# Kernel tuning notes

Measured on AMD Instinct MI355X. Metric: run time of the kernel, lower is better.

## Reference

```python
import jax, jax.numpy as jnp
import numpy as np

N_EMBED = 256
N_HEADS = 4
HEAD_SIZE = N_EMBED // N_HEADS  # 64
BLOCK_SIZE = 768
LN_EPS = 1e-5


def layer_norm(x, g, b):
    mu = jnp.mean(x, axis=-1, keepdims=True)
    var = jnp.var(x, axis=-1, keepdims=True)
    return (x - mu) * jax.lax.rsqrt(var + LN_EPS) * g + b


def setup_inputs() -> dict:
    key = jax.random.key(0)
    ks = jax.random.split(key, 12)
    B, T, C, H, hs = 32, BLOCK_SIZE, N_EMBED, N_HEADS, HEAD_SIZE
    s_in = 1.0 / np.sqrt(C)
    s_ff = 1.0 / np.sqrt(4 * C)
    return {
        "x": jax.random.normal(ks[0], (B, T, C), jnp.float32),
        # per-head projections, stacked: [H, C, hs]
        "Wq": jax.random.normal(ks[1], (H, C, hs), jnp.float32) * s_in,
        "Wk": jax.random.normal(ks[2], (H, C, hs), jnp.float32) * s_in,
        "Wv": jax.random.normal(ks[3], (H, C, hs), jnp.float32) * s_in,
        "Wo": jax.random.normal(ks[4], (C, C), jnp.float32) * s_in,
        "bo": jnp.zeros((C,), jnp.float32),
        "W1": jax.random.normal(ks[5], (C, 4 * C), jnp.float32) * s_in,
        "b1": jnp.zeros((4 * C,), jnp.float32),
        "W2": jax.random.normal(ks[6], (4 * C, C), jnp.float32) * s_ff,
        "b2": jnp.zeros((C,), jnp.float32),
        "g1": jnp.ones((C,), jnp.float32),
        "be1": jnp.zeros((C,), jnp.float32),
        "g2": jnp.ones((C,), jnp.float32),
        "be2": jnp.zeros((C,), jnp.float32),
    }


def reference(x, Wq, Wk, Wv, Wo, bo, W1, b1, W2, b2, g1, be1, g2, be2):
    B, T, C = x.shape
    # --- multi-head causal self-attention (pre-LN) ---
    h = layer_norm(x, g1, be1)
    q = jnp.einsum("btc,hcd->bhtd", h, Wq)
    k = jnp.einsum("btc,hcd->bhtd", h, Wk)
    v = jnp.einsum("btc,hcd->bhtd", h, Wv)
    scores = jnp.einsum("bhtd,bhsd->bhts", q, k) * (HEAD_SIZE ** -0.5)
    causal = jnp.tril(jnp.ones((T, T), bool))
    scores = jnp.where(causal, scores, -jnp.inf)
    attn = jax.nn.softmax(scores, axis=-1)  # dropout = identity (eval)
    o = jnp.einsum("bhts,bhsd->bhtd", attn, v)
    o = o.transpose(0, 2, 1, 3).reshape(B, T, C)  # concat heads
    x = x + o @ Wo + bo
    # --- feed-forward (pre-LN) ---
    h2 = layer_norm(x, g2, be2)
    x = x + jax.nn.relu(h2 @ W1 + b1) @ W2 + b2
    return x
```

## Files before the change

kernel.cpp:

```cpp
#include <hip/hip_runtime.h>
#include <stdint.h>

using short8   = __attribute__((ext_vector_type(8))) short;
using f32x4    = __attribute__((ext_vector_type(4))) float;
using ushort4v = __attribute__((ext_vector_type(4))) unsigned short;
using uint2v   = __attribute__((ext_vector_type(2))) unsigned int;

#define CSC  0.1803368801111f
#define FIXC 20.0f

__device__ __forceinline__ unsigned short f2bf(float f) {
    unsigned int u = __builtin_bit_cast(unsigned int, f);
    u += 0x7FFFu + ((u >> 16) & 1u);
    return (unsigned short)(u >> 16);
}
__device__ __forceinline__ float bf2f(unsigned short s) {
    unsigned int u = ((unsigned int)s) << 16;
    return __builtin_bit_cast(float, u);
}
__device__ __forceinline__ unsigned pk2bf(float a, float b) {
    unsigned r;
    asm("v_cvt_pk_bf16_f32 %0, %1, %2" : "=v"(r) : "v"(a), "v"(b));
    return r;
}

__device__ __forceinline__ void gload16(const void* g, void* l) {
    __builtin_amdgcn_global_load_lds(
        (const __attribute__((address_space(1))) void*)(uintptr_t)g,
        (__attribute__((address_space(3))) void*)(unsigned)(uintptr_t)l,
        16, 0, 0);
}

__device__ __forceinline__ uint2v ln_row_pk(f32x4 v, f32x4 gv, f32x4 bvv) {
    float s  = v[0] + v[1] + v[2] + v[3];
    float s2 = v[0]*v[0] + v[1]*v[1] + v[2]*v[2] + v[3]*v[3];
    for (int m = 1; m < 64; m <<= 1) {
        s  += __shfl_xor(s,  m, 64);
        s2 += __shfl_xor(s2, m, 64);
    }
    float mu  = s * (1.0f / 256.0f);
    float var = s2 * (1.0f / 256.0f) - mu * mu;
    float rs  = rsqrtf(var + 1e-5f);
    float r0 = (v[0] - mu) * rs * gv[0] + bvv[0];
    float r1 = (v[1] - mu) * rs * gv[1] + bvv[1];
    float r2 = (v[2] - mu) * rs * gv[2] + bvv[2];
    float r3 = (v[3] - mu) * rs * gv[3] + bvv[3];
    uint2v u; u[0] = pk2bf(r0, r1); u[1] = pk2bf(r2, r3);
    return u;
}

__global__ __launch_bounds__(256) void prep_k(const float* __restrict__ x, const float* __restrict__ g1,
                                              const float* __restrict__ be1, unsigned short* __restrict__ h,
                                              const float* __restrict__ Wq, const float* __restrict__ Wk,
                                              const float* __restrict__ Wv, const float* __restrict__ Wo,
                                              const float* __restrict__ W1, const float* __restrict__ W2,
                                              unsigned short* __restrict__ wpackT, unsigned short* __restrict__ woT,
                                              unsigned short* __restrict__ w1T, unsigned short* __restrict__ w2T) {
    __shared__ float t[64][65];
    if (blockIdx.x >= 192) {
        int row  = (blockIdx.x - 192) * 4 + (threadIdx.x >> 6);
        int lane = threadIdx.x & 63;
        f32x4 v = *(const f32x4*)(x + (size_t)row * 256 + lane * 4);
        f32x4 gv = *(const f32x4*)(g1 + lane * 4);
        f32x4 bv = *(const f32x4*)(be1 + lane * 4);
        uint2v u = ln_row_pk(v, gv, bv);
        *(uint2v*)(h + (size_t)row * 256 + lane * 4) = u;
        return;
    }
    const int bid = blockIdx.x;
    const float* in; unsigned short* out;
    int R, C, r0, c0;
    if (bid < 48) {
        int z = bid >> 2, cx = bid & 3;
        int qkv = z >> 2, hh = z & 3;
        in = ((qkv == 0) ? Wq : (qkv == 1) ? Wk : Wv) + (size_t)hh * 256 * 64;
        out = wpackT + (size_t)(qkv * 256 + hh * 64) * 256;
        R = 256; C = 64; r0 = cx * 64; c0 = 0;
    } else if (bid < 64) {
        int tt = bid - 48;
        in = Wo; out = woT; R = 256; C = 256; r0 = (tt >> 2) * 64; c0 = (tt & 3) * 64;
    } else if (bid < 128) {
        int tt = bid - 64;
        in = W1; out = w1T; R = 256; C = 1024; r0 = (tt & 3) * 64; c0 = (tt >> 2) * 64;
    } else {
        int tt = bid - 128;
        in = W2; out = w2T; R = 1024; C = 256; r0 = (tt & 15) * 64; c0 = (tt >> 4) * 64;
    }
    const int tx = threadIdx.x & 63, ty = threadIdx.x >> 6;
    #pragma unroll
    for (int i = 0; i < 64; i += 4)
        t[i + ty][tx] = in[(size_t)(r0 + i + ty) * C + c0 + tx];
    __syncthreads();
    #pragma unroll
    for (int i = 0; i < 64; i += 4)
        out[(size_t)(c0 + i + ty) * R + r0 + tx] = f2bf(t[tx][i + ty]);
}

__global__ __launch_bounds__(256) void qkv_k(const unsigned short* __restrict__ h,
                                             const unsigned short* __restrict__ wpackT,
                                             unsigned short* __restrict__ qk,
                                             unsigned short* __restrict__ vT) {
    __shared__ unsigned short As[128 * 64];
    __shared__ unsigned short Bs[128 * 64];
    const int tid  = threadIdx.x;
    const int lane = tid & 63;
    const int w    = tid >> 6;
    const int wm   = w >> 1, wn = w & 1;
    const int l15  = lane & 15, l4 = lane >> 4;
    const int bid  = blockIdx.x;

    const unsigned short *A, *BT;
    unsigned short* outp;
    int bm, bn, N;
    float qsc = 1.0f;
    if (bid < 768) {
        bn = bid & 3;  bm = bid >> 2;
        A = h; BT = wpackT; outp = qk; N = 512;
        if (bn < 2) qsc = CSC;
    } else {
        int t = bid - 768;
        bm = t & 1;    bn = t >> 1;
        A = wpackT + 512 * 256; BT = h; outp = vT; N = 24576;
    }
    const int K = 256;

    f32x4 acc[4][4] = {};

    const size_t K2 = (size_t)K * 2;
    const int i0   = w * 4096 + lane * 16;
    const int row0 = i0 >> 7;
    const int cb0  = (i0 & 127) ^ ((row0 & 7) << 4);
    const char* aSrc = (const char*)A  + ((size_t)(bm * 128 + row0)) * K2 + cb0;
    const char* bSrc = (const char*)BT + ((size_t)(bn * 128 + row0)) * K2 + cb0;

    for (int t = 0; t < 4; ++t) {
        {
            const char* aS = aSrc + (size_t)t * 128;
            const char* bS = bSrc + (size_t)t * 128;
            char* aD = (char*)&As[0] + w * 4096;
            char* bD = (char*)&Bs[0] + w * 4096;
            #pragma unroll
            for (int c = 0; c < 4; ++c) {
                gload16(aS + (size_t)c * 8 * K2, aD + c * 1024);
                gload16(bS + (size_t)c * 8 * K2, bD + c * 1024);
            }
        }
        __syncthreads();
        #pragma unroll
        for (int kf = 0; kf < 2; ++kf) {
            int kb = kf * 64 + l4 * 16;
            short8 af[4], bfr[4];
            #pragma unroll
            for (int mf = 0; mf < 4; ++mf) {
                int row = wm * 64 + mf * 16 + l15;
                af[mf] = *(const short8*)((const char*)&As[0] + ((row * 128 + kb) ^ ((row & 7) << 4)));
            }
            #pragma unroll
            for (int nf = 0; nf < 4; ++nf) {
                int row = wn * 64 + nf * 16 + l15;
                bfr[nf] = *(const short8*)((const char*)&Bs[0] + ((row * 128 + kb) ^ ((row & 7) << 4)));
            }
            #pragma unroll
            for (int mf = 0; mf < 4; ++mf)
                #pragma unroll
                for (int nf = 0; nf < 4; ++nf)
                    acc[mf][nf] = __builtin_amdgcn_mfma_f32_16x16x32_bf16(af[mf], bfr[nf], acc[mf][nf], 0, 0, 0);
        }
        __syncthreads();
    }

    #pragma unroll
    for (int nf = 0; nf < 4; ++nf) {
        int col = bn * 128 + wn * 64 + nf * 16 + l15;
        #pragma unroll
        for (int mf = 0; mf < 4; ++mf) {
            int row0o = bm * 128 + wm * 64 + mf * 16 + l4 * 4;
            size_t off = (size_t)row0o * N + col;
            unsigned p01 = pk2bf(acc[mf][nf][0] * qsc, acc[mf][nf][1] * qsc);
            unsigned p23 = pk2bf(acc[mf][nf][2] * qsc, acc[mf][nf][3] * qsc);
            outp[off]                 = (unsigned short)p01;
            outp[off + (size_t)N]     = (unsigned short)(p01 >> 16);
            outp[off + (size_t)N * 2] = (unsigned short)p23;
            outp[off + (size_t)N * 3] = (unsigned short)(p23 >> 16);
        }
    }
}

template <int EPI, bool DB>
__global__ __launch_bounds__(256) void gemm_bt(const unsigned short* __restrict__ A,
                                               const unsigned short* __restrict__ BT,
                                               void* __restrict__ outp,
                                               const float* __restrict__ bias,
                                               const void* __restrict__ resid,
                                               int K, int N) {
    __shared__ unsigned short As[DB ? 2 : 1][128 * 64];
    __shared__ unsigned short Bs[DB ? 2 : 1][128 * 64];
    const int tid  = threadIdx.x;
    const int lane = tid & 63;
    const int w    = tid >> 6;
    const int wm   = w >> 1, wn = w & 1;
    const int bm   = blockIdx.y, bn = blockIdx.x;
    const int l15  = lane & 15, l4 = lane >> 4;

    f32x4 acc[4][4] = {};

    const size_t K2 = (size_t)K * 2;
    const int i0   = w * 4096 + lane * 16;
    const int row0 = i0 >> 7;
    const int cb0  = (i0 & 127) ^ ((row0 & 7) << 4);
    const char* aSrc = (const char*)A  + ((size_t)(bm * 128 + row0)) * K2 + cb0;
    const char* bSrc = (const char*)BT + ((size_t)(bn * 128 + row0)) * K2 + cb0;
    const int nt = K >> 6;

    auto stage = [&](int t, int buf) {
        const char* aS = aSrc + (size_t)t * 128;
        const char* bS = bSrc + (size_t)t * 128;
        char* aD = (char*)&As[buf][0] + w * 4096;
        char* bD = (char*)&Bs[buf][0] + w * 4096;
        #pragma unroll
        for (int c = 0; c < 4; ++c) {
            gload16(aS + (size_t)c * 8 * K2, aD + c * 1024);
            gload16(bS + (size_t)c * 8 * K2, bD + c * 1024);
        }
    };
    auto compute = [&](int buf) {
        const char* AsB = (const char*)&As[buf][0];
        const char* BsB = (const char*)&Bs[buf][0];
        #pragma unroll
        for (int kf = 0; kf < 2; ++kf) {
            int kb = kf * 64 + l4 * 16;
            short8 af[4], bfr[4];
            #pragma unroll
            for (int mf = 0; mf < 4; ++mf) {
                int row = wm * 64 + mf * 16 + l15;
                af[mf] = *(const short8*)(AsB + ((row * 128 + kb) ^ ((row & 7) << 4)));
            }
            #pragma unroll
            for (int nf = 0; nf < 4; ++nf) {
                int row = wn * 64 + nf * 16 + l15;
                bfr[nf] = *(const short8*)(BsB + ((row * 128 + kb) ^ ((row & 7) << 4)));
            }
            #pragma unroll
            for (int mf = 0; mf < 4; ++mf)
                #pragma unroll
                for (int nf = 0; nf < 4; ++nf)
                    acc[mf][nf] = __builtin_amdgcn_mfma_f32_16x16x32_bf16(af[mf], bfr[nf], acc[mf][nf], 0, 0, 0);
        }
    };

    if (DB) {
        stage(0, 0);
        for (int t = 0; t < nt; ++t) {
            const int cur = t & 1;
            __syncthreads();
            if (t + 1 < nt) stage(t + 1, cur ^ 1);
            compute(cur);
        }
    } else {
        for (int t = 0; t < nt; ++t) {
            stage(t, 0);
            __syncthreads();
            compute(0);
            __syncthreads();
        }
    }

    #pragma unroll
    for (int nf = 0; nf < 4; ++nf) {
        int col = bn * 128 + wn * 64 + nf * 16 + l15;
        float bv = bias[col];
        #pragma unroll
        for (int mf = 0; mf < 4; ++mf) {
            int row0o = bm * 128 + wm * 64 + mf * 16 + l4 * 4;
            size_t off = (size_t)row0o * N + col;
            float v[4];
            #pragma unroll
            for (int r = 0; r < 4; ++r)
                v[r] = acc[mf][nf][r] + bv + ((const float*)resid)[off + (size_t)r * N];
            unsigned short* O = (unsigned short*)outp;
            unsigned p01 = pk2bf(v[0], v[1]), p23 = pk2bf(v[2], v[3]);
            O[off]                 = (unsigned short)p01;
            O[off + (size_t)N]     = (unsigned short)(p01 >> 16);
            O[off + (size_t)N * 2] = (unsigned short)p23;
            O[off + (size_t)N * 3] = (unsigned short)(p23 >> 16);
        }
    }
}

__global__ __launch_bounds__(256) void ff_fused(const unsigned short* __restrict__ x1b,
                                                const float* __restrict__ g2,
                                                const float* __restrict__ be2,
                                                const unsigned short* __restrict__ w1T,
                                                const unsigned short* __restrict__ w2T,
                                                const float* __restrict__ b1,
                                                const float* __restrict__ b2,
                                                float* __restrict__ out) {
    __shared__ unsigned short sA[4][64 * 64];
    __shared__ unsigned short sW[16384];
    __shared__ unsigned short sAct[64 * 64];
    const int tid = threadIdx.x, lane = tid & 63, w = tid >> 6;
    const int l15 = lane & 15, l4 = lane >> 4;
    const int wm = w >> 1, wn = w & 1;
    const int r0 = blockIdx.x * 64;

    {
        f32x4 gv = *(const f32x4*)(g2 + lane * 4);
        f32x4 bv = *(const f32x4*)(be2 + lane * 4);
        const int ks = lane >> 4, colb = (lane & 15) * 8;
        #pragma unroll
        for (int it = 0; it < 16; ++it) {
            int row = it * 4 + w;
            ushort4v u4 = *(const ushort4v*)(x1b + (size_t)(r0 + row) * 256 + lane * 4);
            f32x4 v;
            #pragma unroll
            for (int i = 0; i < 4; ++i) v[i] = bf2f(u4[i]);
            uint2v u = ln_row_pk(v, gv, bv);
            *(uint2v*)((char*)&sA[0][0] + ks * 8192 + row * 128 + (colb ^ ((row & 7) << 4))) = u;
        }
    }

    f32x4 oacc[2][8] = {};

    for (int c = 0; c < 16; ++c) {
        {
            const char* wb = (const char*)w1T + (size_t)(c * 64) * 512;
            #pragma unroll
            for (int g = 0; g < 8; ++g) {
                int j = g * 4096 + tid * 16;
                int ks = j >> 13, row = (j >> 7) & 63, cb = j & 127;
                gload16(wb + (size_t)row * 512 + ks * 128 + (cb ^ ((row & 7) << 4)),
                        (char*)&sW[0] + j);
            }
        }
        __syncthreads();

        f32x4 aacc[2][2] = {};
        __builtin_amdgcn_s_setprio(1);
        #pragma unroll
        for (int ks = 0; ks < 4; ++ks) {
            #pragma unroll
            for (int kf = 0; kf < 2; ++kf) {
                const int kb = kf * 64 + l4 * 16;
                short8 hf[2], wf[2];
                #pragma unroll
                for (int mf = 0; mf < 2; ++mf) {
                    int row = wm * 32 + mf * 16 + l15;
                    hf[mf] = *(const short8*)((const char*)&sA[ks][0] + ((row * 128 + kb) ^ ((row & 7) << 4)));
                }
                #pragma unroll
                for (int nf = 0; nf < 2; ++nf) {
                    int row = wn * 32 + nf * 16 + l15;
                    wf[nf] = *(const short8*)((const char*)&sW[ks * 4096] + ((row * 128 + kb) ^ ((row & 7) << 4)));
                }
                #pragma unroll
                for (int mf = 0; mf < 2; ++mf)
                    #pragma unroll
                    for (int nf = 0; nf < 2; ++nf)
                        aacc[mf][nf] = __builtin_amdgcn_mfma_f32_16x16x32_bf16(wf[nf], hf[mf], aacc[mf][nf], 0, 0, 0);
            }
        }
        __builtin_amdgcn_s_setprio(0);
        #pragma unroll
        for (int mf = 0; mf < 2; ++mf)
            #pragma unroll
            for (int nf = 0; nf < 2; ++nf) {
                int nl = wn * 32 + nf * 16 + l4 * 4;
                f32x4 bv = *(const f32x4*)(b1 + c * 64 + nl);
                float v0 = aacc[mf][nf][0] + bv[0]; v0 = v0 > 0.0f ? v0 : 0.0f;
                float v1 = aacc[mf][nf][1] + bv[1]; v1 = v1 > 0.0f ? v1 : 0.0f;
                float v2 = aacc[mf][nf][2] + bv[2]; v2 = v2 > 0.0f ? v2 : 0.0f;
                float v3 = aacc[mf][nf][3] + bv[3]; v3 = v3 > 0.0f ? v3 : 0.0f;
                uint2v u; u[0] = pk2bf(v0, v1); u[1] = pk2bf(v2, v3);
                int m = wm * 32 + mf * 16 + l15;
                *(uint2v*)((char*)&sAct[0] + ((m * 128 + nl * 2) ^ ((m & 7) << 4))) = u;
            }
        __syncthreads();

        {
            const char* wb = (const char*)w2T + (size_t)c * 128;
            #pragma unroll
            for (int g = 0; g < 8; ++g) {
                int j = g * 4096 + tid * 16;
                int row = j >> 7, cb = j & 127;
                gload16(wb + (size_t)row * 2048 + (cb ^ ((row & 7) << 4)),
                        (char*)&sW[0] + j);
            }
        }
        __syncthreads();

        __builtin_amdgcn_s_setprio(1);
        #pragma unroll
        for (int kf = 0; kf < 2; ++kf) {
            const int kb = kf * 64 + l4 * 16;
            short8 af[2], wf[8];
            #pragma unroll
            for (int mf = 0; mf < 2; ++mf) {
                int row = wm * 32 + mf * 16 + l15;
                af[mf] = *(const short8*)((const char*)&sAct[0] + ((row * 128 + kb) ^ ((row & 7) << 4)));
            }
            #pragma unroll
            for (int nf = 0; nf < 8; ++nf) {
                int row = wn * 128 + nf * 16 + l15;
                wf[nf] = *(const short8*)((const char*)&sW[0] + ((row * 128 + kb) ^ ((row & 7) << 4)));
            }
            #pragma unroll
            for (int mf = 0; mf < 2; ++mf)
                #pragma unroll
                for (int nf = 0; nf < 8; ++nf)
                    oacc[mf][nf] = __builtin_amdgcn_mfma_f32_16x16x32_bf16(af[mf], wf[nf], oacc[mf][nf], 0, 0, 0);
        }
        __builtin_amdgcn_s_setprio(0);
        __syncthreads();
    }

    #pragma unroll
    for (int nf = 0; nf < 8; ++nf) {
        const int col = wn * 128 + nf * 16 + l15;
        const float bv = b2[col];
        #pragma unroll
        for (int mf = 0; mf < 2; ++mf) {
            const int row = r0 + wm * 32 + mf * 16 + l4 * 4;
            const size_t off = (size_t)row * 256 + col;
            #pragma unroll
            for (int r = 0; r < 4; ++r)
                out[off + (size_t)r * 256] = oacc[mf][nf][r] + bv + bf2f(x1b[off + (size_t)r * 256]);
        }
    }
}

__global__ __launch_bounds__(256) void attn_k(const unsigned short* __restrict__ qk,
                                              const unsigned short* __restrict__ vT,
                                              unsigned short* __restrict__ o) {
    __shared__ unsigned short Ks[2][64 * 64];
    __shared__ unsigned short Vt[2][64 * 64];
    __shared__ unsigned short Pl[4][16 * 64];
    const int tid = threadIdx.x, lane = tid & 63, w = tid >> 6;
    const int l15 = lane & 15, l4 = lane >> 4;
    const int gid = blockIdx.x;
    const int xcd = gid & 7, slot = gid >> 3;
    const int sl6 = slot / 6;
    const int bh  = xcd * 16 + sl6;
    const int x   = slot - sl6 * 6;
    const int qb1 = x, qb2 = 11 - x;
    const int b = bh >> 2, h = bh & 3;
    const unsigned short* Qb = qk + (size_t)b * 768 * 512 + h * 64;
    const char* Kg = (const char*)(Qb + 256);
    const char* Vg = (const char*)(vT + (size_t)(h * 64) * 24576 + (size_t)b * 768);
    const int t01 = qb1 * 64, t02 = qb2 * 64;
    const int tq1 = t01 + w * 16 + l15;
    const int tq2 = t02 + w * 16 + l15;

    short8 q1f0 = *(const short8*)(Qb + (size_t)tq1 * 512 + l4 * 8);
    short8 q1f1 = *(const short8*)(Qb + (size_t)tq1 * 512 + 32 + l4 * 8);
    short8 q2f0 = *(const short8*)(Qb + (size_t)tq2 * 512 + l4 * 8);
    short8 q2f1 = *(const short8*)(Qb + (size_t)tq2 * 512 + 32 + l4 * 8);

    const int srow = w * 16 + (lane >> 3);
    const int scb  = ((lane & 7) * 16) ^ ((srow & 7) << 4);
    const char* kSrc = Kg + (size_t)srow * 1024 + scb;
    const char* vSrc = Vg + (size_t)srow * 49152 + scb;
    char* kDst0 = (char*)&Ks[0][0] + w * 2048;
    char* vDst0 = (char*)&Vt[0][0] + w * 2048;

    f32x4 oA[4] = {}, oB[4] = {};
    float lsA = 0.0f, lsB = 0.0f;
    unsigned short* Pw = &Pl[w][0];
    const char* KsB;
    const char* VtB;
    int sb = 0;

    auto do_tile = [&](short8 qf0, short8 qf1, f32x4 (&oacc)[4], float& lsum, bool diag, int tq) {
        f32x4 sacc[4] = {};
        __builtin_amdgcn_s_setprio(1);
        #pragma unroll
        for (int kf = 0; kf < 2; ++kf) {
            const int kb = kf * 64 + l4 * 16;
            short8 qf = kf ? qf1 : qf0;
            #pragma unroll
            for (int nf = 0; nf < 4; ++nf) {
                int sr = nf * 16 + l15;
                short8 kfr = *(const short8*)(KsB + ((sr * 128 + kb) ^ ((sr & 7) << 4)));
                sacc[nf] = __builtin_amdgcn_mfma_f32_16x16x32_bf16(kfr, qf, sacc[nf], 0, 0, 0);
            }
        }
        __builtin_amdgcn_s_setprio(0);

        if (diag) {
            #pragma unroll
            for (int nf = 0; nf < 4; ++nf)
                #pragma unroll
                for (int r = 0; r < 4; ++r) {
                    int s = sb * 64 + nf * 16 + l4 * 4 + r;
                    if (s > tq) sacc[nf][r] = -1e30f;
                }
        }
        float psum = 0.0f;
        #pragma unroll
        for (int nf = 0; nf < 4; ++nf) {
            float p0 = __builtin_amdgcn_exp2f(sacc[nf][0] - FIXC);
            float p1 = __builtin_amdgcn_exp2f(sacc[nf][1] - FIXC);
            float p2 = __builtin_amdgcn_exp2f(sacc[nf][2] - FIXC);
            float p3 = __builtin_amdgcn_exp2f(sacc[nf][3] - FIXC);
            psum += (p0 + p1) + (p2 + p3);
            uint2v u; u[0] = pk2bf(p0, p1); u[1] = pk2bf(p2, p3);
            *(uint2v*)((char*)Pw + ((l15 * 128 + nf * 32 + l4 * 8) ^ ((l15 & 7) << 4))) = u;
        }
        psum += __shfl_xor(psum, 16, 64);
        psum += __shfl_xor(psum, 32, 64);
        lsum += psum;

        __builtin_amdgcn_s_setprio(1);
        #pragma unroll
        for (int kf = 0; kf < 2; ++kf) {
            const int kb = kf * 64 + l4 * 16;
            short8 pa = *(const short8*)((const char*)Pw + ((l15 * 128 + kb) ^ ((l15 & 7) << 4)));
            #pragma unroll
            for (int nf = 0; nf < 4; ++nf) {
                int dr = nf * 16 + l15;
                short8 vfr = *(const short8*)(VtB + ((dr * 128 + kb) ^ ((dr & 7) << 4)));
                oacc[nf] = __builtin_amdgcn_mfma_f32_16x16x32_bf16(pa, vfr, oacc[nf], 0, 0, 0);
            }
        }
        __builtin_amdgcn_s_setprio(0);
    };

    gload16(kSrc, kDst0);                 gload16(kSrc + 8 * 1024, kDst0 + 1024);
    gload16(vSrc, vDst0);                 gload16(vSrc + 8 * 49152, vDst0 + 1024);

    for (sb = 0; sb <= qb2; ++sb) {
        const int pb = sb & 1;
        __syncthreads();
        if (sb < qb2) {
            const char* ks = kSrc + (size_t)(sb + 1) * 65536;
            const char* vs = vSrc + (size_t)(sb + 1) * 128;
            char* kd = kDst0 + (pb ^ 1) * 8192;
            char* vd = vDst0 + (pb ^ 1) * 8192;
            gload16(ks, kd);              gload16(ks + 8 * 1024, kd + 1024);
            gload16(vs, vd);              gload16(vs + 8 * 49152, vd + 1024);
        }
        KsB = (const char*)&Ks[0][0] + pb * 8192;
        VtB = (const char*)&Vt[0][0] + pb * 8192;

        do_tile(q2f0, q2f1, oB, lsB, sb == qb2, tq2);
        if (sb <= qb1) do_tile(q1f0, q1f1, oA, lsA, sb == qb1, tq1);
    }

    float liA = 1.0f / lsA, liB = 1.0f / lsB;
    float lrA[4], lrB[4];
    #pragma unroll
    for (int r = 0; r < 4; ++r) {
        lrA[r] = __shfl(liA, l4 * 4 + r, 64);
        lrB[r] = __shfl(liB, l4 * 4 + r, 64);
    }
    const int tA = t01 + w * 16 + l4 * 4;
    const int tB = t02 + w * 16 + l4 * 4;
    unsigned short* oa = o + ((size_t)(b * 768 + tA)) * 256 + h * 64;
    unsigned short* ob = o + ((size_t)(b * 768 + tB)) * 256 + h * 64;
    #pragma unroll
    for (int nf = 0; nf < 4; ++nf) {
        unsigned a01 = pk2bf(oA[nf][0] * lrA[0], oA[nf][1] * lrA[1]);
        unsigned a23 = pk2bf(oA[nf][2] * lrA[2], oA[nf][3] * lrA[3]);
        unsigned b01 = pk2bf(oB[nf][0] * lrB[0], oB[nf][1] * lrB[1]);
        unsigned b23 = pk2bf(oB[nf][2] * lrB[2], oB[nf][3] * lrB[3]);
        oa[nf * 16 + l15]       = (unsigned short)a01;
        oa[256 + nf * 16 + l15] = (unsigned short)(a01 >> 16);
        oa[512 + nf * 16 + l15] = (unsigned short)a23;
        oa[768 + nf * 16 + l15] = (unsigned short)(a23 >> 16);
        ob[nf * 16 + l15]       = (unsigned short)b01;
        ob[256 + nf * 16 + l15] = (unsigned short)(b01 >> 16);
        ob[512 + nf * 16 + l15] = (unsigned short)b23;
        ob[768 + nf * 16 + l15] = (unsigned short)(b23 >> 16);
    }
}

extern "C" void kernel_launch(void* const* d_in, const int* in_sizes, int n_in,
                              void* d_out, int out_size, void* d_ws, size_t ws_size,
                              hipStream_t stream) {
    const float* x   = (const float*)d_in[0];
    const float* Wq  = (const float*)d_in[1];
    const float* Wk  = (const float*)d_in[2];
    const float* Wv  = (const float*)d_in[3];
    const float* Wo  = (const float*)d_in[4];
    const float* bo  = (const float*)d_in[5];
    const float* W1  = (const float*)d_in[6];
    const float* b1  = (const float*)d_in[7];
    const float* W2  = (const float*)d_in[8];
    const float* b2  = (const float*)d_in[9];
    const float* g1  = (const float*)d_in[10];
    const float* be1 = (const float*)d_in[11];
    const float* g2  = (const float*)d_in[12];
    const float* be2 = (const float*)d_in[13];

    char* ws = (char*)d_ws;
    unsigned short* qk_ws  = (unsigned short*)(ws + 0);
    unsigned short* vT_ws  = (unsigned short*)(ws + 25165824);
    unsigned short* o_ws   = (unsigned short*)(ws + 37748736);
    unsigned short* h_ws   = (unsigned short*)(ws + 50331648);
    unsigned short* x1b_ws = (unsigned short*)(ws + 62914560);
    unsigned short* wpackT = (unsigned short*)(ws + 88080384);
    unsigned short* woT    = (unsigned short*)(ws + 88473600);
    unsigned short* w1T    = (unsigned short*)(ws + 88604672);
    unsigned short* w2T    = (unsigned short*)(ws + 89128960);

    prep_k<<<6336, 256, 0, stream>>>(x, g1, be1, h_ws, Wq, Wk, Wv, Wo, W1, W2, wpackT, woT, w1T, w2T);
    qkv_k<<<1152, 256, 0, stream>>>(h_ws, wpackT, qk_ws, vT_ws);
    attn_k<<<768, 256, 0, stream>>>(qk_ws, vT_ws, o_ws);
    gemm_bt<2, true><<<dim3(2, 192), 256, 0, stream>>>(o_ws, woT, x1b_ws, bo, x, 256, 256);
    ff_fused<<<384, 256, 0, stream>>>(x1b_ws, g2, be2, w1T, w2T, b1, b2, (float*)d_out);
}
```

Measured before the change: 119.1 us.

## Double-buffer QKV GEMM tiles and overlap weight staging in fused FFN

The QKV projection kernel gains double-buffered LDS tiles, so the next K-slice is loaded while the current one is multiplied, with one barrier per iteration instead of two. The fused FFN kernel now splits the hidden dimension into 32-wide chunks with separate W1 and W2 LDS buffers. The W2 load for a chunk overlaps the W1 MFMAs and the next W1 load overlaps the W2 MFMAs, which removes one barrier per chunk. In exchange the QKV kernel uses twice the LDS and the FFN runs twice as many, smaller chunks with less reuse per load.

```diff
diff --git a/kernel.cpp b/kernel.cpp
--- a/kernel.cpp
+++ b/kernel.cpp
@@ -100,8 +100,8 @@
                                              const unsigned short* __restrict__ wpackT,
                                              unsigned short* __restrict__ qk,
                                              unsigned short* __restrict__ vT) {
-    __shared__ unsigned short As[128 * 64];
-    __shared__ unsigned short Bs[128 * 64];
+    __shared__ unsigned short As[2][128 * 64];
+    __shared__ unsigned short Bs[2][128 * 64];
     const int tid  = threadIdx.x;
     const int lane = tid & 63;
     const int w    = tid >> 6;
@@ -133,19 +133,25 @@
     const char* aSrc = (const char*)A  + ((size_t)(bm * 128 + row0)) * K2 + cb0;
     const char* bSrc = (const char*)BT + ((size_t)(bn * 128 + row0)) * K2 + cb0;
 
+    auto stage = [&](int t, int buf) {
+        const char* aS = aSrc + (size_t)t * 128;
+        const char* bS = bSrc + (size_t)t * 128;
+        char* aD = (char*)&As[buf][0] + w * 4096;
+        char* bD = (char*)&Bs[buf][0] + w * 4096;
+        #pragma unroll
+        for (int c = 0; c < 4; ++c) {
+            gload16(aS + (size_t)c * 8 * K2, aD + c * 1024);
+            gload16(bS + (size_t)c * 8 * K2, bD + c * 1024);
+        }
+    };
+
+    stage(0, 0);
     for (int t = 0; t < 4; ++t) {
-        {
-            const char* aS = aSrc + (size_t)t * 128;
-            const char* bS = bSrc + (size_t)t * 128;
-            char* aD = (char*)&As[0] + w * 4096;
-            char* bD = (char*)&Bs[0] + w * 4096;
-            #pragma unroll
-            for (int c = 0; c < 4; ++c) {
-                gload16(aS + (size_t)c * 8 * K2, aD + c * 1024);
-                gload16(bS + (size_t)c * 8 * K2, bD + c * 1024);
-            }
-        }
+        const int cur = t & 1;
         __syncthreads();
+        if (t + 1 < 4) stage(t + 1, cur ^ 1);
+        const char* AsB = (const char*)&As[cur][0];
+        const char* BsB = (const char*)&Bs[cur][0];
         #pragma unroll
         for (int kf = 0; kf < 2; ++kf) {
             int kb = kf * 64 + l4 * 16;
@@ -153,12 +159,12 @@
             #pragma unroll
             for (int mf = 0; mf < 4; ++mf) {
                 int row = wm * 64 + mf * 16 + l15;
-                af[mf] = *(const short8*)((const char*)&As[0] + ((row * 128 + kb) ^ ((row & 7) << 4)));
+                af[mf] = *(const short8*)(AsB + ((row * 128 + kb) ^ ((row & 7) << 4)));
             }
             #pragma unroll
             for (int nf = 0; nf < 4; ++nf) {
                 int row = wn * 64 + nf * 16 + l15;
-                bfr[nf] = *(const short8*)((const char*)&Bs[0] + ((row * 128 + kb) ^ ((row & 7) << 4)));
+                bfr[nf] = *(const short8*)(BsB + ((row * 128 + kb) ^ ((row & 7) << 4)));
             }
             #pragma unroll
             for (int mf = 0; mf < 4; ++mf)
@@ -166,7 +172,6 @@
                 for (int nf = 0; nf < 4; ++nf)
                     acc[mf][nf] = __builtin_amdgcn_mfma_f32_16x16x32_bf16(af[mf], bfr[nf], acc[mf][nf], 0, 0, 0);
         }
-        __syncthreads();
     }
 
     #pragma unroll
@@ -296,8 +301,9 @@
                                                 const float* __restrict__ b2,
                                                 float* __restrict__ out) {
     __shared__ unsigned short sA[4][64 * 64];
-    __shared__ unsigned short sW[16384];
-    __shared__ unsigned short sAct[64 * 64];
+    __shared__ unsigned short sW1[32 * 256];
+    __shared__ unsigned short sW2[256 * 32];
+    __shared__ unsigned short sAct[64 * 32];
     const int tid = threadIdx.x, lane = tid & 63, w = tid >> 6;
     const int l15 = lane & 15, l4 = lane >> 4;
     const int wm = w >> 1, wn = w & 1;
@@ -319,98 +325,91 @@
         }
     }
 
+    auto stage_w1 = [&](int c) {
+        const char* wb = (const char*)w1T + (size_t)(c * 32) * 512;
+        #pragma unroll
+        for (int g = 0; g < 4; ++g) {
+            int j = g * 4096 + tid * 16;
+            int ks = j >> 12, row = (j >> 7) & 31, cb = j & 127;
+            gload16(wb + (size_t)row * 512 + ks * 128 + (cb ^ ((row & 7) << 4)),
+                    (char*)&sW1[0] + j);
+        }
+    };
+    auto stage_w2 = [&](int c) {
+        const char* wb = (const char*)w2T + (size_t)c * 64;
+        #pragma unroll
+        for (int g = 0; g < 4; ++g) {
+            int j = g * 4096 + tid * 16;
+            int row = j >> 6, cb = j & 63;
+            gload16(wb + (size_t)row * 2048 + (cb ^ ((row & 3) << 4)),
+                    (char*)&sW2[0] + j);
+        }
+    };
+
+    stage_w1(0);
     f32x4 oacc[2][8] = {};
 
-    for (int c = 0; c < 16; ++c) {
-        {
-            const char* wb = (const char*)w1T + (size_t)(c * 64) * 512;
-            #pragma unroll
-            for (int g = 0; g < 8; ++g) {
-                int j = g * 4096 + tid * 16;
-                int ks = j >> 13, row = (j >> 7) & 63, cb = j & 127;
-                gload16(wb + (size_t)row * 512 + ks * 128 + (cb ^ ((row & 7) << 4)),
-                        (char*)&sW[0] + j);
-            }
-        }
+    for (int c = 0; c < 32; ++c) {
         __syncthreads();
 
-        f32x4 aacc[2][2] = {};
+        stage_w2(c);
+
+        f32x4 aacc[2] = {};
         __builtin_amdgcn_s_setprio(1);
         #pragma unroll
         for (int ks = 0; ks < 4; ++ks) {
             #pragma unroll
             for (int kf = 0; kf < 2; ++kf) {
                 const int kb = kf * 64 + l4 * 16;
-                short8 hf[2], wf[2];
+                int wrow = wn * 16 + l15;
+                short8 wf = *(const short8*)((const char*)&sW1[0] + ks * 4096
+                              + ((wrow * 128 + kb) ^ ((wrow & 7) << 4)));
                 #pragma unroll
                 for (int mf = 0; mf < 2; ++mf) {
-                    int row = wm * 32 + mf * 16 + l15;
-                    hf[mf] = *(const short8*)((const char*)&sA[ks][0] + ((row * 128 + kb) ^ ((row & 7) << 4)));
+                    int hrow = wm * 32 + mf * 16 + l15;
+                    short8 hf = *(const short8*)((const char*)&sA[0][0] + ks * 8192
+                                  + ((hrow * 128 + kb) ^ ((hrow & 7) << 4)));
+                    aacc[mf] = __builtin_amdgcn_mfma_f32_16x16x32_bf16(wf, hf, aacc[mf], 0, 0, 0);
                 }
-                #pragma unroll
-                for (int nf = 0; nf < 2; ++nf) {
-                    int row = wn * 32 + nf * 16 + l15;
-                    wf[nf] = *(const short8*)((const char*)&sW[ks * 4096] + ((row * 128 + kb) ^ ((row & 7) << 4)));
-                }
+            }
+        }
+        __builtin_amdgcn_s_setprio(0);
+        #pragma unroll
+        for (int mf = 0; mf < 2; ++mf) {
+            int nl = wn * 16 + l4 * 4;
+            f32x4 bv = *(const f32x4*)(b1 + c * 32 + nl);
+            float v0 = aacc[mf][0] + bv[0]; v0 = v0 > 0.0f ? v0 : 0.0f;
+            float v1 = aacc[mf][1] + bv[1]; v1 = v1 > 0.0f ? v1 : 0.0f;
+            float v2 = aacc[mf][2] + bv[2]; v2 = v2 > 0.0f ? v2 : 0.0f;
+            float v3 = aacc[mf][3] + bv[3]; v3 = v3 > 0.0f ? v3 : 0.0f;
+            uint2v u; u[0] = pk2bf(v0, v1); u[1] = pk2bf(v2, v3);
+            int m = wm * 32 + mf * 16 + l15;
+            *(uint2v*)((char*)&sAct[0] + m * 64 + ((nl * 2) ^ ((m & 3) << 4))) = u;
+        }
+
+        __syncthreads();
+
+        if (c + 1 < 32) stage_w1(c + 1);
+
+        __builtin_amdgcn_s_setprio(1);
+        {
+            const int kb = l4 * 16;
+            short8 af[2];
+            #pragma unroll
+            for (int mf = 0; mf < 2; ++mf) {
+                int m = wm * 32 + mf * 16 + l15;
+                af[mf] = *(const short8*)((const char*)&sAct[0] + m * 64 + (kb ^ ((m & 3) << 4)));
+            }
+            #pragma unroll
+            for (int nf = 0; nf < 8; ++nf) {
+                int n2 = wn * 128 + nf * 16 + l15;
+                short8 wf = *(const short8*)((const char*)&sW2[0] + n2 * 64 + (kb ^ ((n2 & 3) << 4)));
                 #pragma unroll
                 for (int mf = 0; mf < 2; ++mf)
-                    #pragma unroll
-                    for (int nf = 0; nf < 2; ++nf)
-                        aacc[mf][nf] = __builtin_amdgcn_mfma_f32_16x16x32_bf16(wf[nf], hf[mf], aacc[mf][nf], 0, 0, 0);
+                    oacc[mf][nf] = __builtin_amdgcn_mfma_f32_16x16x32_bf16(af[mf], wf, oacc[mf][nf], 0, 0, 0);
             }
         }
         __builtin_amdgcn_s_setprio(0);
-        #pragma unroll
-        for (int mf = 0; mf < 2; ++mf)
-            #pragma unroll
-            for (int nf = 0; nf < 2; ++nf) {
-                int nl = wn * 32 + nf * 16 + l4 * 4;
-                f32x4 bv = *(const f32x4*)(b1 + c * 64 + nl);
-                float v0 = aacc[mf][nf][0] + bv[0]; v0 = v0 > 0.0f ? v0 : 0.0f;
-                float v1 = aacc[mf][nf][1] + bv[1]; v1 = v1 > 0.0f ? v1 : 0.0f;
-                float v2 = aacc[mf][nf][2] + bv[2]; v2 = v2 > 0.0f ? v2 : 0.0f;
-                float v3 = aacc[mf][nf][3] + bv[3]; v3 = v3 > 0.0f ? v3 : 0.0f;
-                uint2v u; u[0] = pk2bf(v0, v1); u[1] = pk2bf(v2, v3);
-                int m = wm * 32 + mf * 16 + l15;
-                *(uint2v*)((char*)&sAct[0] + ((m * 128 + nl * 2) ^ ((m & 7) << 4))) = u;
-            }
-        __syncthreads();
-
-        {
-            const char* wb = (const char*)w2T + (size_t)c * 128;
-            #pragma unroll
-            for (int g = 0; g < 8; ++g) {
-                int j = g * 4096 + tid * 16;
-                int row = j >> 7, cb = j & 127;
-                gload16(wb + (size_t)row * 2048 + (cb ^ ((row & 7) << 4)),
-                        (char*)&sW[0] + j);
-            }
-        }
-        __syncthreads();
-
-        __builtin_amdgcn_s_setprio(1);
-        #pragma unroll
-        for (int kf = 0; kf < 2; ++kf) {
-            const int kb = kf * 64 + l4 * 16;
-            short8 af[2], wf[8];
-            #pragma unroll
-            for (int mf = 0; mf < 2; ++mf) {
-                int row = wm * 32 + mf * 16 + l15;
-                af[mf] = *(const short8*)((const char*)&sAct[0] + ((row * 128 + kb) ^ ((row & 7) << 4)));
-            }
-            #pragma unroll
-            for (int nf = 0; nf < 8; ++nf) {
-                int row = wn * 128 + nf * 16 + l15;
-                wf[nf] = *(const short8*)((const char*)&sW[0] + ((row * 128 + kb) ^ ((row & 7) << 4)));
-            }
-            #pragma unroll
-            for (int mf = 0; mf < 2; ++mf)
-                #pragma unroll
-                for (int nf = 0; nf < 8; ++nf)
-                    oacc[mf][nf] = __builtin_amdgcn_mfma_f32_16x16x32_bf16(af[mf], wf[nf], oacc[mf][nf], 0, 0, 0);
-        }
-        __builtin_amdgcn_s_setprio(0);
-        __syncthreads();
     }
 
     #pragma unroll
```

Result: no change. 121.0 us (+1.7%).
